# Kernel optimization log

Hardware: AMD Instinct MI355X
Metric: run time of the kernel (lower is better)

Reference implementation:

```python
import jax, jax.numpy as jnp
import numpy as np

N = 50000      # nodes
E = 800000     # edges (before self-loops)
IN = 128       # input_dim
HID = 64       # hidden_dim
EMB = 32       # embedding_dim
HEADS = 4
NEG_SLOPE = 0.2
BN_EPS = 1e-5


def setup_inputs() -> dict:
    key = jax.random.key(0)
    ks = jax.random.split(key, 20)
    s = 0.1
    x = jax.random.normal(ks[0], (N, IN), jnp.float32)
    edge_index = jax.random.randint(ks[1], (2, E), 0, N, dtype=jnp.int64)
    # GAT layer 0: 128 -> 64, 4 heads, concat
    W0 = jax.random.normal(ks[2], (IN, HEADS * HID), jnp.float32) * s
    a_src0 = jax.random.normal(ks[3], (HEADS, HID), jnp.float32) * s
    a_dst0 = jax.random.normal(ks[4], (HEADS, HID), jnp.float32) * s
    b0 = jax.random.normal(ks[5], (HEADS * HID,), jnp.float32) * s
    # BatchNorm1d(256) in eval mode (running stats)
    bn_gamma = jax.random.uniform(ks[6], (HEADS * HID,), jnp.float32, 0.5, 1.5)
    bn_beta = jax.random.normal(ks[7], (HEADS * HID,), jnp.float32) * s
    bn_mean = jax.random.normal(ks[8], (HEADS * HID,), jnp.float32) * s
    bn_var = jax.random.uniform(ks[9], (HEADS * HID,), jnp.float32, 0.5, 1.5)
    # GAT layer 1: 256 -> 32, 1 head, mean (concat=False)
    W1 = jax.random.normal(ks[10], (HEADS * HID, EMB), jnp.float32) * s
    a_src1 = jax.random.normal(ks[11], (1, EMB), jnp.float32) * s
    a_dst1 = jax.random.normal(ks[12], (1, EMB), jnp.float32) * s
    b1 = jax.random.normal(ks[13], (EMB,), jnp.float32) * s
    # prediction head: Linear(32,64) -> ReLU -> Linear(64,1)
    head_W1 = jax.random.normal(ks[14], (EMB, HID), jnp.float32) * s
    head_b1 = jax.random.normal(ks[15], (HID,), jnp.float32) * s
    head_W2 = jax.random.normal(ks[16], (HID, 1), jnp.float32) * s
    head_b2 = jax.random.normal(ks[17], (1,), jnp.float32) * s
    return dict(x=x, edge_index=edge_index, W0=W0, a_src0=a_src0, a_dst0=a_dst0, b0=b0,
                bn_gamma=bn_gamma, bn_beta=bn_beta, bn_mean=bn_mean, bn_var=bn_var,
                W1=W1, a_src1=a_src1, a_dst1=a_dst1, b1=b1,
                head_W1=head_W1, head_b1=head_b1, head_W2=head_W2, head_b2=head_b2)


def _gat_conv(x, src, dst, W, a_src, a_dst, bias, heads, out_c, concat):
    # PyG GATConv (eval mode, dropout off, self-loops already in src/dst)
    n = x.shape[0]
    h = (x @ W).reshape(n, heads, out_c)                # [N,H,C]
    alpha_s = jnp.sum(h * a_src, axis=-1)               # [N,H]
    alpha_d = jnp.sum(h * a_dst, axis=-1)               # [N,H]
    e = alpha_s[src] + alpha_d[dst]                      # [Etot,H]
    e = jnp.where(e > 0, e, NEG_SLOPE * e)               # leaky_relu
    m = jax.ops.segment_max(e, dst, num_segments=n)      # softmax over incoming edges
    e = jnp.exp(e - m[dst])
    denom = jax.ops.segment_sum(e, dst, num_segments=n)
    alpha = e / denom[dst]                               # [Etot,H]; self-loops ensure denom>0
    out = jax.ops.segment_sum(h[src] * alpha[:, :, None], dst, num_segments=n)  # [N,H,C]
    out = out.reshape(n, heads * out_c) if concat else out.mean(axis=1)
    return out + bias


def reference(x, edge_index, W0, a_src0, a_dst0, b0,
              bn_gamma, bn_beta, bn_mean, bn_var,
              W1, a_src1, a_dst1, b1,
              head_W1, head_b1, head_W2, head_b2):
    n = x.shape[0]
    loops = jnp.arange(n, dtype=edge_index.dtype)
    src = jnp.concatenate([edge_index[0], loops])
    dst = jnp.concatenate([edge_index[1], loops])

    h = _gat_conv(x, src, dst, W0, a_src0, a_dst0, b0, HEADS, HID, True)   # [N,256]
    h = (h - bn_mean) * (bn_gamma / jnp.sqrt(bn_var + BN_EPS)) + bn_beta   # BN eval
    h = jax.nn.relu(h)                                                      # dropout off (eval)
    node_embeddings = _gat_conv(h, src, dst, W1, a_src1, a_dst1, b1, 1, EMB, False)  # [N,32]

    graph_embedding = jnp.mean(node_embeddings, axis=0, keepdims=True)      # [1,32]
    hid = jax.nn.relu(graph_embedding @ head_W1 + head_b1)
    predictions = hid @ head_W2 + head_b2                                    # [1,1]
    return node_embeddings, predictions
```

## Files before the change

kernel.cpp:

```cpp
#include <hip/hip_runtime.h>


#define NEG_SLOPE 0.2f
#define BN_EPS 1e-5f
#define LOG2E 1.4426950408889634f

typedef __attribute__((ext_vector_type(8))) short bf16x8;
typedef __attribute__((ext_vector_type(4))) float f32x4;

__device__ __forceinline__ float bf2f(unsigned short u) {
  return __uint_as_float((unsigned)u << 16);
}
__device__ __forceinline__ unsigned short f2bf(float f) {
  unsigned u = __float_as_uint(f);
  u += 0x7fff + ((u >> 16) & 1);
  return (unsigned short)(u >> 16);
}

__global__ __launch_bounds__(256) void w_swizzle_kernel(
    const float* __restrict__ W0, const float* __restrict__ W1,
    unsigned short* __restrict__ w0sw, unsigned short* __restrict__ w1sw) {
  int o = blockIdx.x * 256 + threadIdx.x;
  if (o < 32768) {
    int j = o & 7, l = (o >> 3) & 63, ks = (o >> 9) & 3,
        ci = (o >> 11) & 3, h = (o >> 13) & 3;
    int row = ks * 32 + (l >> 4) * 8 + j;
    int col = h * 64 + ci * 16 + (l & 15);
    w0sw[o] = f2bf(W0[row * 256 + col]);
  } else if (o < 40960) {
    int o2 = o - 32768;
    int j = o2 & 7, l = (o2 >> 3) & 63, ks = (o2 >> 9) & 7, ci = (o2 >> 12) & 1;
    int row = ks * 32 + (l >> 4) * 8 + j;
    int col = ci * 16 + (l & 15);
    w1sw[o2] = f2bf(W1[row * 32 + col]);
  }
}

__global__ __launch_bounds__(256) void gemm0_mfma_kernel(
    const float* __restrict__ x, const unsigned short* __restrict__ w0sw,
    const float* __restrict__ a_src0, const float* __restrict__ a_dst0,
    unsigned short* __restrict__ h0bf, float* __restrict__ as0,
    float* __restrict__ ad0, int M) {
  __shared__ unsigned short Asw[16 * 64 * 8];
  const int t = threadIdx.x;
  const int lane = t & 63;
  const int h = t >> 6;
  const int row0 = blockIdx.x * 64;

  #pragma unroll
  for (int i = 0; i < 8; ++i) {
    int q = t + 256 * i;
    int r = q >> 5, c4 = q & 31;
    int gr = row0 + r;
    float4 v = make_float4(0.f, 0.f, 0.f, 0.f);
    if (gr < M) v = *reinterpret_cast<const float4*>(&x[(size_t)gr * 128 + c4 * 4]);
    int ks = c4 >> 3;
    int lane_hi = (c4 >> 1) & 3;
    int j0 = (c4 & 1) * 4;
    int slot = (r >> 4) * 4 + ks;
    int dlane = (r & 15) + 16 * lane_hi;
    ushort4 o;
    o.x = f2bf(v.x); o.y = f2bf(v.y); o.z = f2bf(v.z); o.w = f2bf(v.w);
    *reinterpret_cast<ushort4*>(&Asw[(slot * 64 + dlane) * 8 + j0]) = o;
  }
  __syncthreads();

  f32x4 acc[4][4] = {};
  const bf16x8* wp = reinterpret_cast<const bf16x8*>(w0sw);
  #pragma unroll
  for (int ks = 0; ks < 4; ++ks) {
    bf16x8 bfrag[4];
    #pragma unroll
    for (int ci = 0; ci < 4; ++ci)
      bfrag[ci] = wp[(h * 16 + ci * 4 + ks) * 64 + lane];
    #pragma unroll
    for (int ri = 0; ri < 4; ++ri) {
      bf16x8 af = *reinterpret_cast<const bf16x8*>(&Asw[((ri * 4 + ks) * 64 + lane) * 8]);
      #pragma unroll
      for (int ci = 0; ci < 4; ++ci)
        acc[ri][ci] = __builtin_amdgcn_mfma_f32_16x16x32_bf16(af, bfrag[ci], acc[ri][ci], 0, 0, 0);
    }
  }

  float av[4], dv[4];
  #pragma unroll
  for (int ci = 0; ci < 4; ++ci) {
    av[ci] = a_src0[h * 64 + ci * 16 + (lane & 15)];
    dv[ci] = a_dst0[h * 64 + ci * 16 + (lane & 15)];
  }
  const int mrow = (lane >> 4) * 4;
  #pragma unroll
  for (int ri = 0; ri < 4; ++ri) {
    #pragma unroll
    for (int r = 0; r < 4; ++r) {
      int gr = row0 + ri * 16 + mrow + r;
      float ps = acc[ri][0][r] * av[0] + acc[ri][1][r] * av[1] +
                 acc[ri][2][r] * av[2] + acc[ri][3][r] * av[3];
      float pd = acc[ri][0][r] * dv[0] + acc[ri][1][r] * dv[1] +
                 acc[ri][2][r] * dv[2] + acc[ri][3][r] * dv[3];
      #pragma unroll
      for (int off = 1; off < 16; off <<= 1) {
        ps += __shfl_xor(ps, off);
        pd += __shfl_xor(pd, off);
      }
      if (gr < M) {
        #pragma unroll
        for (int ci = 0; ci < 4; ++ci)
          h0bf[(size_t)gr * 256 + h * 64 + ci * 16 + (lane & 15)] = f2bf(acc[ri][ci][r]);
        if ((lane & 15) == 0) { as0[gr * 4 + h] = ps * LOG2E; ad0[gr * 4 + h] = pd * LOG2E; }
      }
    }
  }
}

__global__ __launch_bounds__(256) void hist_kernel(
    const int* __restrict__ dsts, int* __restrict__ deg, int E, int N) {
  int e = blockIdx.x * 256 + threadIdx.x;
  if (e >= E + N) return;
  int d = (e < E) ? dsts[e] : e - E;
  atomicAdd(&deg[d], 1);
}

__global__ __launch_bounds__(256) void scan_block_kernel(
    const int* __restrict__ deg, int* __restrict__ excl,
    int* __restrict__ bsum, int N) {
  __shared__ int tmp[256];
  int i = blockIdx.x * 256 + threadIdx.x;
  int v = (i < N) ? deg[i] : 0;
  tmp[threadIdx.x] = v;
  __syncthreads();
  #pragma unroll
  for (int off = 1; off < 256; off <<= 1) {
    int t = (threadIdx.x >= off) ? tmp[threadIdx.x - off] : 0;
    __syncthreads();
    tmp[threadIdx.x] += t;
    __syncthreads();
  }
  if (i < N) excl[i] = tmp[threadIdx.x] - v;
  if (threadIdx.x == 255) bsum[blockIdx.x] = tmp[255];
}

__global__ __launch_bounds__(256) void scan_add_kernel(
    int* __restrict__ rowptr, const int* __restrict__ bsum,
    int* __restrict__ cursor, int N, int Etot) {
  __shared__ int wred[4];
  const int t = threadIdx.x;
  int v = (t < blockIdx.x) ? bsum[t] : 0;
  #pragma unroll
  for (int off = 32; off >= 1; off >>= 1) v += __shfl_xor(v, off);
  if ((t & 63) == 0) wred[t >> 6] = v;
  __syncthreads();
  const int prefix = wred[0] + wred[1] + wred[2] + wred[3];
  int i = blockIdx.x * 256 + t;
  if (i < N) {
    int r = rowptr[i] + prefix;
    rowptr[i] = r;
    cursor[i] = r;
  }
  if (i == 0) rowptr[N] = Etot;
}

__global__ __launch_bounds__(256) void scatter_kernel(
    const int* __restrict__ srcs, const int* __restrict__ dsts,
    int* __restrict__ cursor, int* __restrict__ csr_src, int E, int N) {
  int e = blockIdx.x * 256 + threadIdx.x;
  if (e >= E + N) return;
  int s, d;
  if (e < E) { s = srcs[e]; d = dsts[e]; } else { s = d = e - E; }
  int pos = atomicAdd(&cursor[d], 1);
  csr_src[pos] = s;
}

__global__ __launch_bounds__(256) void agg0_kernel(
    const int* __restrict__ rowptr, const int* __restrict__ csr_src,
    const unsigned short* __restrict__ h0bf, const float* __restrict__ as0,
    const float* __restrict__ ad0, const float* __restrict__ b0,
    const float* __restrict__ gamma, const float* __restrict__ beta,
    const float* __restrict__ mean, const float* __restrict__ var,
    const unsigned short* __restrict__ w1sw,
    const float* __restrict__ a_src1, const float* __restrict__ a_dst1,
    unsigned short* __restrict__ h1bf, float* __restrict__ as1,
    float* __restrict__ ad1, int N) {
  __shared__ float wlds[4][64];
  __shared__ unsigned short Asw2[8 * 64 * 8];
  const int lane = threadIdx.x & 63;
  const int wid = threadIdx.x >> 6;
  const int n = blockIdx.x * 4 + wid;
  const bool valid = n < N;
  const int h = lane >> 4;
  const int eidx = lane & 15;
  const int bb = lane & 48;

  if (valid) {
    const int beg = rowptr[n], end = rowptr[n + 1];
    const float adv = ad0[n * 4 + h];
    float4 acc = make_float4(0.f, 0.f, 0.f, 0.f);
    float wsum = 0.f;

    for (int i = beg; i < end; i += 16) {
      const int rem = end - i;
      const int ne = rem < 16 ? rem : 16;
      const int li = (eidx < ne) ? eidx : (ne - 1);
      const int src = csr_src[i + li];
      float xx = as0[(unsigned)(src * 4 + h)] + adv;
      xx = fmaxf(xx, NEG_SLOPE * xx);
      float wl = (eidx < ne) ? exp2f(xx) : 0.f;
      wsum += wl;
      wlds[wid][lane] = wl;
      int e = 0;
      for (; e + 8 <= ne; e += 8) {
        const int s0 = __builtin_amdgcn_readlane(src, e + 0);
        const int s1 = __builtin_amdgcn_readlane(src, e + 1);
        const int s2 = __builtin_amdgcn_readlane(src, e + 2);
        const int s3 = __builtin_amdgcn_readlane(src, e + 3);
        const int s4 = __builtin_amdgcn_readlane(src, e + 4);
        const int s5 = __builtin_amdgcn_readlane(src, e + 5);
        const int s6 = __builtin_amdgcn_readlane(src, e + 6);
        const int s7 = __builtin_amdgcn_readlane(src, e + 7);
        ushort4 v0 = *reinterpret_cast<const ushort4*>(&(h0bf + (size_t)s0 * 256)[lane * 4]);
        ushort4 v1 = *reinterpret_cast<const ushort4*>(&(h0bf + (size_t)s1 * 256)[lane * 4]);
        ushort4 v2 = *reinterpret_cast<const ushort4*>(&(h0bf + (size_t)s2 * 256)[lane * 4]);
        ushort4 v3 = *reinterpret_cast<const ushort4*>(&(h0bf + (size_t)s3 * 256)[lane * 4]);
        ushort4 v4 = *reinterpret_cast<const ushort4*>(&(h0bf + (size_t)s4 * 256)[lane * 4]);
        ushort4 v5 = *reinterpret_cast<const ushort4*>(&(h0bf + (size_t)s5 * 256)[lane * 4]);
        ushort4 v6 = *reinterpret_cast<const ushort4*>(&(h0bf + (size_t)s6 * 256)[lane * 4]);
        ushort4 v7 = *reinterpret_cast<const ushort4*>(&(h0bf + (size_t)s7 * 256)[lane * 4]);
        const float w0 = wlds[wid][bb + e + 0];
        const float w1 = wlds[wid][bb + e + 1];
        const float w2 = wlds[wid][bb + e + 2];
        const float w3 = wlds[wid][bb + e + 3];
        const float w4 = wlds[wid][bb + e + 4];
        const float w5 = wlds[wid][bb + e + 5];
        const float w6 = wlds[wid][bb + e + 6];
        const float w7 = wlds[wid][bb + e + 7];
        acc.x += ((w0 * bf2f(v0.x) + w1 * bf2f(v1.x)) + (w2 * bf2f(v2.x) + w3 * bf2f(v3.x))) +
                 ((w4 * bf2f(v4.x) + w5 * bf2f(v5.x)) + (w6 * bf2f(v6.x) + w7 * bf2f(v7.x)));
        acc.y += ((w0 * bf2f(v0.y) + w1 * bf2f(v1.y)) + (w2 * bf2f(v2.y) + w3 * bf2f(v3.y))) +
                 ((w4 * bf2f(v4.y) + w5 * bf2f(v5.y)) + (w6 * bf2f(v6.y) + w7 * bf2f(v7.y)));
        acc.z += ((w0 * bf2f(v0.z) + w1 * bf2f(v1.z)) + (w2 * bf2f(v2.z) + w3 * bf2f(v3.z))) +
                 ((w4 * bf2f(v4.z) + w5 * bf2f(v5.z)) + (w6 * bf2f(v6.z) + w7 * bf2f(v7.z)));
        acc.w += ((w0 * bf2f(v0.w) + w1 * bf2f(v1.w)) + (w2 * bf2f(v2.w) + w3 * bf2f(v3.w))) +
                 ((w4 * bf2f(v4.w) + w5 * bf2f(v5.w)) + (w6 * bf2f(v6.w) + w7 * bf2f(v7.w)));
      }
      for (; e < ne; ++e) {
        const int s0 = __builtin_amdgcn_readlane(src, e);
        const float w0 = wlds[wid][bb + e];
        ushort4 v = *reinterpret_cast<const ushort4*>(&(h0bf + (size_t)s0 * 256)[lane * 4]);
        acc.x += w0 * bf2f(v.x); acc.y += w0 * bf2f(v.y);
        acc.z += w0 * bf2f(v.z); acc.w += w0 * bf2f(v.w);
      }
    }

    #pragma unroll
    for (int off = 1; off < 16; off <<= 1) wsum += __shfl_xor(wsum, off);

    const float inv = 1.0f / wsum;
    const int j = lane * 4;
    float4 bbv = *reinterpret_cast<const float4*>(&b0[j]);
    float4 mu = *reinterpret_cast<const float4*>(&mean[j]);
    float4 gg = *reinterpret_cast<const float4*>(&gamma[j]);
    float4 vv = *reinterpret_cast<const float4*>(&var[j]);
    float4 be = *reinterpret_cast<const float4*>(&beta[j]);
    float4 o;
    o.x = (acc.x * inv + bbv.x - mu.x) * (gg.x * rsqrtf(vv.x + BN_EPS)) + be.x;
    o.y = (acc.y * inv + bbv.y - mu.y) * (gg.y * rsqrtf(vv.y + BN_EPS)) + be.y;
    o.z = (acc.z * inv + bbv.z - mu.z) * (gg.z * rsqrtf(vv.z + BN_EPS)) + be.z;
    o.w = (acc.w * inv + bbv.w - mu.w) * (gg.w * rsqrtf(vv.w + BN_EPS)) + be.w;
    ushort4 ob;
    ob.x = f2bf(fmaxf(o.x, 0.f)); ob.y = f2bf(fmaxf(o.y, 0.f));
    ob.z = f2bf(fmaxf(o.z, 0.f)); ob.w = f2bf(fmaxf(o.w, 0.f));
    const int ks = lane >> 3;
    const int lane_hi = (lane >> 1) & 3;
    const int j0 = (lane & 1) * 4;
    const int dlane = wid + 16 * lane_hi;
    *reinterpret_cast<ushort4*>(&Asw2[(ks * 64 + dlane) * 8 + j0]) = ob;
  }
  __syncthreads();

  if (wid == 0) {
    const bf16x8* bp = reinterpret_cast<const bf16x8*>(w1sw);
    f32x4 c0 = {}, c1 = {};
    #pragma unroll
    for (int ks = 0; ks < 8; ++ks) {
      bf16x8 af = *reinterpret_cast<const bf16x8*>(&Asw2[(ks * 64 + lane) * 8]);
      c0 = __builtin_amdgcn_mfma_f32_16x16x32_bf16(af, bp[(0 * 8 + ks) * 64 + lane], c0, 0, 0, 0);
      c1 = __builtin_amdgcn_mfma_f32_16x16x32_bf16(af, bp[(1 * 8 + ks) * 64 + lane], c1, 0, 0, 0);
    }
    const float av0 = a_src1[lane & 15], av1 = a_src1[16 + (lane & 15)];
    const float dv0 = a_dst1[lane & 15], dv1 = a_dst1[16 + (lane & 15)];
    const int rowgrp = lane >> 4;
    #pragma unroll
    for (int r = 0; r < 4; ++r) {
      float ps = c0[r] * av0 + c1[r] * av1;
      float pd = c0[r] * dv0 + c1[r] * dv1;
      #pragma unroll
      for (int off = 1; off < 16; off <<= 1) {
        ps += __shfl_xor(ps, off);
        pd += __shfl_xor(pd, off);
      }
      const int gn = blockIdx.x * 4 + r;
      if (rowgrp == 0 && gn < N) {
        h1bf[(size_t)gn * 32 + (lane & 15)]      = f2bf(c0[r]);
        h1bf[(size_t)gn * 32 + 16 + (lane & 15)] = f2bf(c1[r]);
        if ((lane & 15) == 0) { as1[gn] = ps * LOG2E; ad1[gn] = pd * LOG2E; }
      }
    }
  }
}

__global__ __launch_bounds__(256) void agg1_kernel(
    const int* __restrict__ rowptr, const int* __restrict__ csr_src,
    const unsigned short* __restrict__ h1bf, const float* __restrict__ as1,
    const float* __restrict__ ad1, const float* __restrict__ b1,
    float* __restrict__ out, int N) {
  __shared__ float wslab[4][16];
  __shared__ int sslab[4][16];
  const int t = threadIdx.x;
  const int lane = t & 63;
  const int wid = t >> 6;
  const int n = blockIdx.x * 4 + wid;
  if (n >= N) return;
  const int c = lane & 31;
  const int half = lane >> 5;
  const int beg = rowptr[n], end = rowptr[n + 1];
  const float adv = ad1[n];
  float acc = 0.f, wsum = 0.f;

  for (int i = beg; i < end; i += 16) {
    int ne = end - i; if (ne > 16) ne = 16;
    if (lane < 16) {
      const int idx = lane < ne ? lane : ne - 1;
      const int s = csr_src[i + idx];
      const float x = as1[s] + adv;
      const float wl = (lane < ne) ? exp2f(fmaxf(x, NEG_SLOPE * x)) : 0.f;
      wslab[wid][lane] = wl;
      sslab[wid][lane] = s;
      wsum += wl;
    }
    for (int e = 0; e < ne; e += 8) {
      const int i0 = e + half, i1 = e + 2 + half, i2 = e + 4 + half, i3 = e + 6 + half;
      const int s0 = sslab[wid][i0], s1 = sslab[wid][i1],
                s2 = sslab[wid][i2], s3 = sslab[wid][i3];
      const float w0 = wslab[wid][i0], w1 = wslab[wid][i1],
                  w2 = wslab[wid][i2], w3 = wslab[wid][i3];
      const unsigned short u0 = h1bf[(size_t)s0 * 32 + c];
      const unsigned short u1 = h1bf[(size_t)s1 * 32 + c];
      const unsigned short u2 = h1bf[(size_t)s2 * 32 + c];
      const unsigned short u3 = h1bf[(size_t)s3 * 32 + c];
      acc += (w0 * bf2f(u0) + w1 * bf2f(u1)) + (w2 * bf2f(u2) + w3 * bf2f(u3));
    }
  }
  #pragma unroll
  for (int off = 1; off < 16; off <<= 1) wsum += __shfl_xor(wsum, off);
  wsum = __shfl(wsum, lane & 15);
  acc += __shfl_xor(acc, 32);
  if (half == 0) out[(size_t)n * 32 + c] = acc / wsum + b1[c];
}

__global__ __launch_bounds__(256) void gsum_kernel(
    const float* __restrict__ out, float* __restrict__ gsum,
    int* __restrict__ ticket,
    const float* __restrict__ hW1, const float* __restrict__ hb1,
    const float* __restrict__ hW2, const float* __restrict__ hb2,
    float* __restrict__ pout, int N) {
  __shared__ float red[8][32];
  __shared__ int lastblk;
  const int t = threadIdx.x;
  const int c = t & 31;
  float s = 0.f;
  const size_t total = (size_t)N * 32;
  for (size_t j = (size_t)blockIdx.x * 256 + t; j < total;
       j += (size_t)gridDim.x * 256)
    s += out[j];
  red[t >> 5][c] = s;
  __syncthreads();
  if (t < 32) {
    float v = 0.f;
    #pragma unroll
    for (int i = 0; i < 8; ++i) v += red[i][t];
    atomicAdd(&gsum[t], v);
  }
  __threadfence();
  if (t == 0) {
    int old = __hip_atomic_fetch_add(ticket, 1, __ATOMIC_ACQ_REL,
                                     __HIP_MEMORY_SCOPE_AGENT);
    lastblk = (old == (int)gridDim.x - 1);
  }
  __syncthreads();
  if (lastblk && t < 64) {
    float invN = 1.0f / (float)N;
    float acc = hb1[t];
    #pragma unroll
    for (int cc = 0; cc < 32; ++cc) {
      float gv = __hip_atomic_load(&gsum[cc], __ATOMIC_RELAXED,
                                   __HIP_MEMORY_SCOPE_AGENT);
      acc += (gv * invN) * hW1[cc * 64 + t];
    }
    acc = fmaxf(acc, 0.f);
    float v = acc * hW2[t];
    #pragma unroll
    for (int off = 1; off < 64; off <<= 1) v += __shfl_xor(v, off);
    if (t == 0) pout[(size_t)N * 32] = v + hb2[0];
  }
}

extern "C" void kernel_launch(void* const* d_in, const int* in_sizes, int n_in,
                              void* d_out, int out_size, void* d_ws, size_t ws_size,
                              hipStream_t stream) {
  const float* x       = (const float*)d_in[0];
  const int*   ei      = (const int*)d_in[1];
  const float* W0      = (const float*)d_in[2];
  const float* a_src0  = (const float*)d_in[3];
  const float* a_dst0  = (const float*)d_in[4];
  const float* b0      = (const float*)d_in[5];
  const float* bn_g    = (const float*)d_in[6];
  const float* bn_b    = (const float*)d_in[7];
  const float* bn_m    = (const float*)d_in[8];
  const float* bn_v    = (const float*)d_in[9];
  const float* W1      = (const float*)d_in[10];
  const float* a_src1  = (const float*)d_in[11];
  const float* a_dst1  = (const float*)d_in[12];
  const float* b1      = (const float*)d_in[13];
  const float* hW1     = (const float*)d_in[14];
  const float* hb1     = (const float*)d_in[15];
  const float* hW2     = (const float*)d_in[16];
  const float* hb2     = (const float*)d_in[17];

  const int N = in_sizes[0] / 128;
  const int E = in_sizes[1] / 2;
  const int Etot = E + N;
  const int* srcs = ei;
  const int* dsts = ei + E;
  const int NB = (N + 255) / 256;

  float* out = (float*)d_out;

  float* ws = (float*)d_ws;
  size_t off = 0;
  unsigned short* h0bf   = (unsigned short*)(ws + off); off += (size_t)N * 128;
  unsigned short* h1bf   = (unsigned short*)(ws + off); off += (size_t)N * 16;
  unsigned short* w0sw   = (unsigned short*)(ws + off); off += 16384;
  unsigned short* w1sw   = (unsigned short*)(ws + off); off += 4096;
  float* as0    = ws + off; off += (size_t)N * 4;
  float* ad0    = ws + off; off += (size_t)N * 4;
  float* as1    = ws + off; off += (size_t)N;
  float* ad1    = ws + off; off += (size_t)N;
  int* rowptr   = (int*)(ws + off); off += (size_t)N + 1;
  int* cursor   = (int*)(ws + off); off += (size_t)N;
  int* bsum     = (int*)(ws + off); off += 256;
  int* csr_src  = (int*)(ws + off); off += (size_t)Etot;
  size_t zoff = off;
  int* deg      = (int*)(ws + off); off += (size_t)N;
  float* gsum   = ws + off; off += 32;
  int* ticket   = (int*)(ws + off); off += 1;

  hipMemsetAsync(ws + zoff, 0, (off - zoff) * sizeof(float), stream);

  auto cdiv = [](long a, long b) { return (int)((a + b - 1) / b); };

  hist_kernel<<<cdiv(Etot, 256), 256, 0, stream>>>(dsts, deg, E, N);
  scan_block_kernel<<<NB, 256, 0, stream>>>(deg, rowptr, bsum, N);
  scan_add_kernel<<<NB, 256, 0, stream>>>(rowptr, bsum, cursor, N, Etot);
  scatter_kernel<<<cdiv(Etot, 256), 256, 0, stream>>>(srcs, dsts, cursor, csr_src, E, N);

  w_swizzle_kernel<<<160, 256, 0, stream>>>(W0, W1, w0sw, w1sw);

  gemm0_mfma_kernel<<<cdiv(N, 64), 256, 0, stream>>>(
      x, w0sw, a_src0, a_dst0, h0bf, as0, ad0, N);
  agg0_kernel<<<cdiv(N, 4), 256, 0, stream>>>(
      rowptr, csr_src, h0bf, as0, ad0, b0, bn_g, bn_b, bn_m, bn_v,
      w1sw, a_src1, a_dst1, h1bf, as1, ad1, N);

  agg1_kernel<<<cdiv(N, 4), 256, 0, stream>>>(rowptr, csr_src, h1bf, as1, ad1,
                                              b1, out, N);

  gsum_kernel<<<128, 256, 0, stream>>>(out, gsum, ticket, hW1, hb1, hW2, hb2, out, N);
}
```

Baseline: 251.3 us.

## Process 16 nodes per block in agg0 with prefetched edge indices and 16-wide gather

Each block of agg0 now handles 16 nodes, four per wavefront in sequence, so every MFMA projection to layer 1 fills all 16 rows instead of 4 and the grid is four times smaller. Inside the edge loop, the next chunk's source indices and attention logits are fetched before the current chunk's gathers are consumed, hiding index-load latency. Full 16-edge chunks take a fully unrolled 16-load gather path for more memory-level parallelism. The cost is higher register pressure from 16 outstanding loads and less parallelism per node, since each wave now walks four nodes serially.

```diff
diff --git a/kernel.cpp b/kernel.cpp
--- a/kernel.cpp
+++ b/kernel.cpp
@@ -185,69 +185,144 @@
   __shared__ unsigned short Asw2[8 * 64 * 8];
   const int lane = threadIdx.x & 63;
   const int wid = threadIdx.x >> 6;
-  const int n = blockIdx.x * 4 + wid;
-  const bool valid = n < N;
+  const int nb = blockIdx.x * 16;
   const int h = lane >> 4;
   const int eidx = lane & 15;
   const int bb = lane & 48;
 
-  if (valid) {
+  #pragma unroll 1
+  for (int k = 0; k < 4; ++k) {
+    const int n = nb + wid * 4 + k;
+    if (n >= N) break;
     const int beg = rowptr[n], end = rowptr[n + 1];
+    const int deg0 = end - beg;
     const float adv = ad0[n * 4 + h];
     float4 acc = make_float4(0.f, 0.f, 0.f, 0.f);
     float wsum = 0.f;
 
-    for (int i = beg; i < end; i += 16) {
-      const int rem = end - i;
-      const int ne = rem < 16 ? rem : 16;
-      const int li = (eidx < ne) ? eidx : (ne - 1);
-      const int src = csr_src[i + li];
-      float xx = as0[(unsigned)(src * 4 + h)] + adv;
+    int i = beg;
+    int ne = deg0 < 16 ? deg0 : 16;
+    int src = csr_src[i + (eidx < ne ? eidx : ne - 1)];
+    float xraw = as0[(unsigned)(src * 4 + h)];
+
+    #pragma unroll 1
+    while (i < end) {
+      float xx = xraw + adv;
       xx = fmaxf(xx, NEG_SLOPE * xx);
       float wl = (eidx < ne) ? exp2f(xx) : 0.f;
       wsum += wl;
       wlds[wid][lane] = wl;
-      int e = 0;
-      for (; e + 8 <= ne; e += 8) {
-        const int s0 = __builtin_amdgcn_readlane(src, e + 0);
-        const int s1 = __builtin_amdgcn_readlane(src, e + 1);
-        const int s2 = __builtin_amdgcn_readlane(src, e + 2);
-        const int s3 = __builtin_amdgcn_readlane(src, e + 3);
-        const int s4 = __builtin_amdgcn_readlane(src, e + 4);
-        const int s5 = __builtin_amdgcn_readlane(src, e + 5);
-        const int s6 = __builtin_amdgcn_readlane(src, e + 6);
-        const int s7 = __builtin_amdgcn_readlane(src, e + 7);
-        ushort4 v0 = *reinterpret_cast<const ushort4*>(&(h0bf + (size_t)s0 * 256)[lane * 4]);
-        ushort4 v1 = *reinterpret_cast<const ushort4*>(&(h0bf + (size_t)s1 * 256)[lane * 4]);
-        ushort4 v2 = *reinterpret_cast<const ushort4*>(&(h0bf + (size_t)s2 * 256)[lane * 4]);
-        ushort4 v3 = *reinterpret_cast<const ushort4*>(&(h0bf + (size_t)s3 * 256)[lane * 4]);
-        ushort4 v4 = *reinterpret_cast<const ushort4*>(&(h0bf + (size_t)s4 * 256)[lane * 4]);
-        ushort4 v5 = *reinterpret_cast<const ushort4*>(&(h0bf + (size_t)s5 * 256)[lane * 4]);
-        ushort4 v6 = *reinterpret_cast<const ushort4*>(&(h0bf + (size_t)s6 * 256)[lane * 4]);
-        ushort4 v7 = *reinterpret_cast<const ushort4*>(&(h0bf + (size_t)s7 * 256)[lane * 4]);
-        const float w0 = wlds[wid][bb + e + 0];
-        const float w1 = wlds[wid][bb + e + 1];
-        const float w2 = wlds[wid][bb + e + 2];
-        const float w3 = wlds[wid][bb + e + 3];
-        const float w4 = wlds[wid][bb + e + 4];
-        const float w5 = wlds[wid][bb + e + 5];
-        const float w6 = wlds[wid][bb + e + 6];
-        const float w7 = wlds[wid][bb + e + 7];
-        acc.x += ((w0 * bf2f(v0.x) + w1 * bf2f(v1.x)) + (w2 * bf2f(v2.x) + w3 * bf2f(v3.x))) +
-                 ((w4 * bf2f(v4.x) + w5 * bf2f(v5.x)) + (w6 * bf2f(v6.x) + w7 * bf2f(v7.x)));
-        acc.y += ((w0 * bf2f(v0.y) + w1 * bf2f(v1.y)) + (w2 * bf2f(v2.y) + w3 * bf2f(v3.y))) +
-                 ((w4 * bf2f(v4.y) + w5 * bf2f(v5.y)) + (w6 * bf2f(v6.y) + w7 * bf2f(v7.y)));
-        acc.z += ((w0 * bf2f(v0.z) + w1 * bf2f(v1.z)) + (w2 * bf2f(v2.z) + w3 * bf2f(v3.z))) +
-                 ((w4 * bf2f(v4.z) + w5 * bf2f(v5.z)) + (w6 * bf2f(v6.z) + w7 * bf2f(v7.z)));
-        acc.w += ((w0 * bf2f(v0.w) + w1 * bf2f(v1.w)) + (w2 * bf2f(v2.w) + w3 * bf2f(v3.w))) +
-                 ((w4 * bf2f(v4.w) + w5 * bf2f(v5.w)) + (w6 * bf2f(v6.w) + w7 * bf2f(v7.w)));
+      const int srccur = src;
+      const int necur = ne;
+      i += 16;
+      const bool more = (i < end);
+      {
+        const int ip = more ? i : beg;
+        const int dd = more ? (end - i) : deg0;
+        ne = dd < 16 ? dd : 16;
+        src = csr_src[ip + (eidx < ne ? eidx : ne - 1)];
       }
-      for (; e < ne; ++e) {
-        const int s0 = __builtin_amdgcn_readlane(src, e);
-        const float w0 = wlds[wid][bb + e];
-        ushort4 v = *reinterpret_cast<const ushort4*>(&(h0bf + (size_t)s0 * 256)[lane * 4]);
-        acc.x += w0 * bf2f(v.x); acc.y += w0 * bf2f(v.y);
-        acc.z += w0 * bf2f(v.z); acc.w += w0 * bf2f(v.w);
+      if (necur == 16) {
+        const int s0  = __builtin_amdgcn_readlane(srccur, 0);
+        const int s1  = __builtin_amdgcn_readlane(srccur, 1);
+        const int s2  = __builtin_amdgcn_readlane(srccur, 2);
+        const int s3  = __builtin_amdgcn_readlane(srccur, 3);
+        const int s4  = __builtin_amdgcn_readlane(srccur, 4);
+        const int s5  = __builtin_amdgcn_readlane(srccur, 5);
+        const int s6  = __builtin_amdgcn_readlane(srccur, 6);
+        const int s7  = __builtin_amdgcn_readlane(srccur, 7);
+        const int s8  = __builtin_amdgcn_readlane(srccur, 8);
+        const int s9  = __builtin_amdgcn_readlane(srccur, 9);
+        const int s10 = __builtin_amdgcn_readlane(srccur, 10);
+        const int s11 = __builtin_amdgcn_readlane(srccur, 11);
+        const int s12 = __builtin_amdgcn_readlane(srccur, 12);
+        const int s13 = __builtin_amdgcn_readlane(srccur, 13);
+        const int s14 = __builtin_amdgcn_readlane(srccur, 14);
+        const int s15 = __builtin_amdgcn_readlane(srccur, 15);
+        ushort4 v0  = *reinterpret_cast<const ushort4*>(&(h0bf + (size_t)s0  * 256)[lane * 4]);
+        ushort4 v1  = *reinterpret_cast<const ushort4*>(&(h0bf + (size_t)s1  * 256)[lane * 4]);
+        ushort4 v2  = *reinterpret_cast<const ushort4*>(&(h0bf + (size_t)s2  * 256)[lane * 4]);
+        ushort4 v3  = *reinterpret_cast<const ushort4*>(&(h0bf + (size_t)s3  * 256)[lane * 4]);
+        ushort4 v4  = *reinterpret_cast<const ushort4*>(&(h0bf + (size_t)s4  * 256)[lane * 4]);
+        ushort4 v5  = *reinterpret_cast<const ushort4*>(&(h0bf + (size_t)s5  * 256)[lane * 4]);
+        ushort4 v6  = *reinterpret_cast<const ushort4*>(&(h0bf + (size_t)s6  * 256)[lane * 4]);
+        ushort4 v7  = *reinterpret_cast<const ushort4*>(&(h0bf + (size_t)s7  * 256)[lane * 4]);
+        ushort4 v8  = *reinterpret_cast<const ushort4*>(&(h0bf + (size_t)s8  * 256)[lane * 4]);
+        ushort4 v9  = *reinterpret_cast<const ushort4*>(&(h0bf + (size_t)s9  * 256)[lane * 4]);
+        ushort4 v10 = *reinterpret_cast<const ushort4*>(&(h0bf + (size_t)s10 * 256)[lane * 4]);
+        ushort4 v11 = *reinterpret_cast<const ushort4*>(&(h0bf + (size_t)s11 * 256)[lane * 4]);
+        ushort4 v12 = *reinterpret_cast<const ushort4*>(&(h0bf + (size_t)s12 * 256)[lane * 4]);
+        ushort4 v13 = *reinterpret_cast<const ushort4*>(&(h0bf + (size_t)s13 * 256)[lane * 4]);
+        ushort4 v14 = *reinterpret_cast<const ushort4*>(&(h0bf + (size_t)s14 * 256)[lane * 4]);
+        ushort4 v15 = *reinterpret_cast<const ushort4*>(&(h0bf + (size_t)s15 * 256)[lane * 4]);
+        xraw = as0[(unsigned)(src * 4 + h)];
+        const float w0  = wlds[wid][bb + 0],  w1  = wlds[wid][bb + 1];
+        const float w2  = wlds[wid][bb + 2],  w3  = wlds[wid][bb + 3];
+        const float w4  = wlds[wid][bb + 4],  w5  = wlds[wid][bb + 5];
+        const float w6  = wlds[wid][bb + 6],  w7  = wlds[wid][bb + 7];
+        const float w8  = wlds[wid][bb + 8],  w9  = wlds[wid][bb + 9];
+        const float w10 = wlds[wid][bb + 10], w11 = wlds[wid][bb + 11];
+        const float w12 = wlds[wid][bb + 12], w13 = wlds[wid][bb + 13];
+        const float w14 = wlds[wid][bb + 14], w15 = wlds[wid][bb + 15];
+        acc.x += (((w0 * bf2f(v0.x) + w1 * bf2f(v1.x)) + (w2 * bf2f(v2.x) + w3 * bf2f(v3.x))) +
+                  ((w4 * bf2f(v4.x) + w5 * bf2f(v5.x)) + (w6 * bf2f(v6.x) + w7 * bf2f(v7.x)))) +
+                 (((w8 * bf2f(v8.x) + w9 * bf2f(v9.x)) + (w10 * bf2f(v10.x) + w11 * bf2f(v11.x))) +
+                  ((w12 * bf2f(v12.x) + w13 * bf2f(v13.x)) + (w14 * bf2f(v14.x) + w15 * bf2f(v15.x))));
+        acc.y += (((w0 * bf2f(v0.y) + w1 * bf2f(v1.y)) + (w2 * bf2f(v2.y) + w3 * bf2f(v3.y))) +
+                  ((w4 * bf2f(v4.y) + w5 * bf2f(v5.y)) + (w6 * bf2f(v6.y) + w7 * bf2f(v7.y)))) +
+                 (((w8 * bf2f(v8.y) + w9 * bf2f(v9.y)) + (w10 * bf2f(v10.y) + w11 * bf2f(v11.y))) +
+                  ((w12 * bf2f(v12.y) + w13 * bf2f(v13.y)) + (w14 * bf2f(v14.y) + w15 * bf2f(v15.y))));
+        acc.z += (((w0 * bf2f(v0.z) + w1 * bf2f(v1.z)) + (w2 * bf2f(v2.z) + w3 * bf2f(v3.z))) +
+                  ((w4 * bf2f(v4.z) + w5 * bf2f(v5.z)) + (w6 * bf2f(v6.z) + w7 * bf2f(v7.z)))) +
+                 (((w8 * bf2f(v8.z) + w9 * bf2f(v9.z)) + (w10 * bf2f(v10.z) + w11 * bf2f(v11.z))) +
+                  ((w12 * bf2f(v12.z) + w13 * bf2f(v13.z)) + (w14 * bf2f(v14.z) + w15 * bf2f(v15.z))));
+        acc.w += (((w0 * bf2f(v0.w) + w1 * bf2f(v1.w)) + (w2 * bf2f(v2.w) + w3 * bf2f(v3.w))) +
+                  ((w4 * bf2f(v4.w) + w5 * bf2f(v5.w)) + (w6 * bf2f(v6.w) + w7 * bf2f(v7.w)))) +
+                 (((w8 * bf2f(v8.w) + w9 * bf2f(v9.w)) + (w10 * bf2f(v10.w) + w11 * bf2f(v11.w))) +
+                  ((w12 * bf2f(v12.w) + w13 * bf2f(v13.w)) + (w14 * bf2f(v14.w) + w15 * bf2f(v15.w))));
+      } else {
+        int e = 0;
+        if (necur >= 8) {
+          const int s0 = __builtin_amdgcn_readlane(srccur, 0);
+          const int s1 = __builtin_amdgcn_readlane(srccur, 1);
+          const int s2 = __builtin_amdgcn_readlane(srccur, 2);
+          const int s3 = __builtin_amdgcn_readlane(srccur, 3);
+          const int s4 = __builtin_amdgcn_readlane(srccur, 4);
+          const int s5 = __builtin_amdgcn_readlane(srccur, 5);
+          const int s6 = __builtin_amdgcn_readlane(srccur, 6);
+          const int s7 = __builtin_amdgcn_readlane(srccur, 7);
+          ushort4 v0 = *reinterpret_cast<const ushort4*>(&(h0bf + (size_t)s0 * 256)[lane * 4]);
+          ushort4 v1 = *reinterpret_cast<const ushort4*>(&(h0bf + (size_t)s1 * 256)[lane * 4]);
+          ushort4 v2 = *reinterpret_cast<const ushort4*>(&(h0bf + (size_t)s2 * 256)[lane * 4]);
+          ushort4 v3 = *reinterpret_cast<const ushort4*>(&(h0bf + (size_t)s3 * 256)[lane * 4]);
+          ushort4 v4 = *reinterpret_cast<const ushort4*>(&(h0bf + (size_t)s4 * 256)[lane * 4]);
+          ushort4 v5 = *reinterpret_cast<const ushort4*>(&(h0bf + (size_t)s5 * 256)[lane * 4]);
+          ushort4 v6 = *reinterpret_cast<const ushort4*>(&(h0bf + (size_t)s6 * 256)[lane * 4]);
+          ushort4 v7 = *reinterpret_cast<const ushort4*>(&(h0bf + (size_t)s7 * 256)[lane * 4]);
+          xraw = as0[(unsigned)(src * 4 + h)];
+          const float w0 = wlds[wid][bb + 0], w1 = wlds[wid][bb + 1];
+          const float w2 = wlds[wid][bb + 2], w3 = wlds[wid][bb + 3];
+          const float w4 = wlds[wid][bb + 4], w5 = wlds[wid][bb + 5];
+          const float w6 = wlds[wid][bb + 6], w7 = wlds[wid][bb + 7];
+          acc.x += ((w0 * bf2f(v0.x) + w1 * bf2f(v1.x)) + (w2 * bf2f(v2.x) + w3 * bf2f(v3.x))) +
+                   ((w4 * bf2f(v4.x) + w5 * bf2f(v5.x)) + (w6 * bf2f(v6.x) + w7 * bf2f(v7.x)));
+          acc.y += ((w0 * bf2f(v0.y) + w1 * bf2f(v1.y)) + (w2 * bf2f(v2.y) + w3 * bf2f(v3.y))) +
+                   ((w4 * bf2f(v4.y) + w5 * bf2f(v5.y)) + (w6 * bf2f(v6.y) + w7 * bf2f(v7.y)));
+          acc.z += ((w0 * bf2f(v0.z) + w1 * bf2f(v1.z)) + (w2 * bf2f(v2.z) + w3 * bf2f(v3.z))) +
+                   ((w4 * bf2f(v4.z) + w5 * bf2f(v5.z)) + (w6 * bf2f(v6.z) + w7 * bf2f(v7.z)));
+          acc.w += ((w0 * bf2f(v0.w) + w1 * bf2f(v1.w)) + (w2 * bf2f(v2.w) + w3 * bf2f(v3.w))) +
+                   ((w4 * bf2f(v4.w) + w5 * bf2f(v5.w)) + (w6 * bf2f(v6.w) + w7 * bf2f(v7.w)));
+          e = 8;
+        } else {
+          xraw = as0[(unsigned)(src * 4 + h)];
+        }
+        for (; e < necur; ++e) {
+          const int s0 = __builtin_amdgcn_readlane(srccur, e);
+          const float w0 = wlds[wid][bb + e];
+          ushort4 v = *reinterpret_cast<const ushort4*>(&(h0bf + (size_t)s0 * 256)[lane * 4]);
+          acc.x += w0 * bf2f(v.x); acc.y += w0 * bf2f(v.y);
+          acc.z += w0 * bf2f(v.z); acc.w += w0 * bf2f(v.w);
+        }
       }
     }
 
@@ -269,10 +344,11 @@
     ushort4 ob;
     ob.x = f2bf(fmaxf(o.x, 0.f)); ob.y = f2bf(fmaxf(o.y, 0.f));
     ob.z = f2bf(fmaxf(o.z, 0.f)); ob.w = f2bf(fmaxf(o.w, 0.f));
+    const int row = wid * 4 + k;
     const int ks = lane >> 3;
     const int lane_hi = (lane >> 1) & 3;
     const int j0 = (lane & 1) * 4;
-    const int dlane = wid + 16 * lane_hi;
+    const int dlane = row + 16 * lane_hi;
     *reinterpret_cast<ushort4*>(&Asw2[(ks * 64 + dlane) * 8 + j0]) = ob;
   }
   __syncthreads();
@@ -288,7 +364,6 @@
     }
     const float av0 = a_src1[lane & 15], av1 = a_src1[16 + (lane & 15)];
     const float dv0 = a_dst1[lane & 15], dv1 = a_dst1[16 + (lane & 15)];
-    const int rowgrp = lane >> 4;
     #pragma unroll
     for (int r = 0; r < 4; ++r) {
       float ps = c0[r] * av0 + c1[r] * av1;
@@ -298,8 +373,8 @@
         ps += __shfl_xor(ps, off);
         pd += __shfl_xor(pd, off);
       }
-      const int gn = blockIdx.x * 4 + r;
-      if (rowgrp == 0 && gn < N) {
+      const int gn = nb + (lane >> 4) * 4 + r;
+      if (gn < N) {
         h1bf[(size_t)gn * 32 + (lane & 15)]      = f2bf(c0[r]);
         h1bf[(size_t)gn * 32 + 16 + (lane & 15)] = f2bf(c1[r]);
         if ((lane & 15) == 0) { as1[gn] = ps * LOG2E; ad1[gn] = pd * LOG2E; }
@@ -467,7 +542,7 @@
 
   gemm0_mfma_kernel<<<cdiv(N, 64), 256, 0, stream>>>(
       x, w0sw, a_src0, a_dst0, h0bf, as0, ad0, N);
-  agg0_kernel<<<cdiv(N, 4), 256, 0, stream>>>(
+  agg0_kernel<<<cdiv(N, 16), 256, 0, stream>>>(
       rowptr, csr_src, h0bf, as0, ad0, b0, bn_g, bn_b, bn_m, bn_v,
       w1sw, a_src1, a_dst1, h1bf, as1, ad1, N);
 
```

Measured after the change: 258.5 us. 1.03x slower.
